# Optimization experiments

Hardware: AMD Instinct MI355X
Metric: run time of the kernel (lower is better)

Reference implementation:

```python
import jax, jax.numpy as jnp
import numpy as np

B, C_IN, C_OUT = 8, 64, 64
H, W = 256, 256
FH, FW = 16, 16  # patch grid from weight map spatial dims
HYPER_PARAMS = C_OUT * C_IN  # kernel_size=1, groups=1


def setup_inputs() -> dict:
    key = jax.random.key(0)
    kx, ks = jax.random.split(key)
    x = jax.random.normal(kx, (B, C_IN, H, W), dtype=jnp.float32)
    # s is the hypernetwork-generated per-patch weight map [b, out*in, fh, fw]
    s = jax.random.normal(ks, (B, HYPER_PARAMS, FH, FW), dtype=jnp.float32)
    return {"x": x, "s": s}


def reference(x, s):
    b, c, h, w = x.shape
    fh, fw = s.shape[-2], s.shape[-1]
    ph, pw = h // fh, w // fw
    out_ch = s.shape[1] // c  # hyper_params = out_ch * c (1x1 kernel, groups=1)
    # weight.permute(0,2,3,1).reshape(b*fh*fw*out, in, 1, 1) -> per-patch [out, in]
    Wp = jnp.transpose(s, (0, 2, 3, 1)).reshape(b, fh, fw, out_ch, c)
    # x.view(b,c,fh,ph,fw,pw).permute(0,2,4,1,3,5) -> per-patch blocks [b,fh,fw,c,ph,pw]
    xp = jnp.transpose(x.reshape(b, c, fh, ph, fw, pw), (0, 2, 4, 1, 3, 5))
    # grouped 1x1 conv over b*fh*fw groups == batched small matmul per patch
    y = jnp.einsum('bijoc,bijcpq->bijopq', Wp, xp)
    # .view(b,fh,fw,-1,ph,pw).permute(0,3,1,4,2,5).reshape(b,-1,h,w)
    return jnp.transpose(y, (0, 3, 1, 4, 2, 5)).reshape(b, out_ch, h, w)
```

## Files before the change

### kernel.cpp

```cpp
#include <hip/hip_runtime.h>

#define NB 8
#define FH 16
#define FW 16

typedef __bf16 bf16x8 __attribute__((ext_vector_type(8)));
typedef float  f32x4  __attribute__((ext_vector_type(4)));

#define WS_BYTES ((size_t)NB * 256 * 512 * 16)

__global__ __launch_bounds__(256) void pack_w_kernel(
    const float* __restrict__ s, bf16x8* __restrict__ ws)
{
    __shared__ float lds[16 * 513];
    const int bid = blockIdx.x;
    const int b   = bid & 7;
    const int pi  = (bid >> 3) & 15;
    const int mt  = (bid >> 7) & 3;
    const int kk  = (bid >> 9) & 1;
    const int tid = threadIdx.x;

    #pragma unroll
    for (int pass = 0; pass < 8; ++pass) {
        const int idx   = pass * 256 + tid;
        const int u     = idx >> 2;
        const int pj4   = idx & 3;
        const int row16 = u >> 5;
        const int cc    = u & 31;
        const size_t row = (size_t)b * 4096 + mt * 1024 + row16 * 64 + kk * 32 + cc;
        const float4 v = *reinterpret_cast<const float4*>(
            s + row * 256 + pi * 16 + pj4 * 4);
        lds[(pj4 * 4 + 0) * 513 + cc * 16 + row16] = v.x;
        lds[(pj4 * 4 + 1) * 513 + cc * 16 + row16] = v.y;
        lds[(pj4 * 4 + 2) * 513 + cc * 16 + row16] = v.z;
        lds[(pj4 * 4 + 3) * 513 + cc * 16 + row16] = v.w;
    }
    __syncthreads();

    const int gl     = tid & 63;
    const int row16  = gl & 15;
    const int lanehi = gl >> 4;
    #pragma unroll
    for (int pjblk = 0; pjblk < 4; ++pjblk) {
        const int pj = pjblk * 4 + (tid >> 6);
        bf16x8 e;
        #pragma unroll
        for (int j = 0; j < 8; ++j)
            e[j] = (__bf16)lds[pj * 513 + (lanehi * 8 + j) * 16 + row16];
        ws[((size_t)(b * 256 + pi * 16 + pj)) * 512 + (mt * 2 + kk) * 64 + gl] = e;
    }
}

__global__ __launch_bounds__(256, 4) void gemm_kernel(
    const float* __restrict__ x,
    const bf16x8* __restrict__ ws,
    float* __restrict__ out)
{
    __shared__ char smem[32768];
    float* smemf = (float*)smem;

    const int bid = blockIdx.x;
    const int b   = bid & 7;
    const int pi  = (bid >> 3) & 15;
    const int ph  = (bid >> 7) & 1;
    const int pjp = (bid >> 8) & 7;
    const int t   = threadIdx.x;
    const int lane = t & 63;
    const int wv   = t >> 6;
    const int pat  = wv & 1;
    const int wrow = wv >> 1;
    const int q    = lane & 15;
    const int hi   = lane >> 4;
    const int w0   = pjp * 32;
    const int row0 = pi * 16 + ph * 8;

    const bf16x8* wbase = ws + ((size_t)(b * 256 + pi * 16 + pjp * 2 + pat)) * 512;
    bf16x8 a[4][2];
    #pragma unroll
    for (int mt = 0; mt < 4; ++mt)
        #pragma unroll
        for (int kk = 0; kk < 2; ++kk)
            a[mt][kk] = wbase[(mt * 2 + kk) * 64 + lane];

    {
        const int swq = lane & 7;
        const int sco = lane >> 3;
        #pragma unroll
        for (int pp = 0; pp < 2; ++pp) {
            const int p = wv * 2 + pp;
            const float* xp = x + ((size_t)(b * 64 + sco * 8)) * 65536
                                + (size_t)(row0 + p) * 256 + w0 + swq * 4;
            f32x4 v[8];
            #pragma unroll
            for (int cc = 0; cc < 8; ++cc)
                v[cc] = *(const f32x4*)(xp + (size_t)cc * 65536);
            #pragma unroll
            for (int i = 0; i < 4; ++i) {
                const int w = swq * 4 + i;
                bf16x8 e;
                #pragma unroll
                for (int cc = 0; cc < 8; ++cc)
                    e[cc] = (__bf16)v[cc][i];
                *(bf16x8*)(smem + p * 4096 + w * 128
                           + ((sco * 16) ^ ((w & 7) << 4) ^ ((p & 7) << 4))) = e;
            }
        }
    }
    __syncthreads();

    bf16x8 bfrag[4][2];
    #pragma unroll
    for (int nt = 0; nt < 4; ++nt) {
        const int p = wrow * 4 + nt;
        const int w = pat * 16 + q;
        #pragma unroll
        for (int kk = 0; kk < 2; ++kk) {
            const int co = kk * 4 + hi;
            bfrag[nt][kk] = *(const bf16x8*)(smem + p * 4096 + w * 128
                            + ((co * 16) ^ ((w & 7) << 4) ^ ((p & 7) << 4)));
        }
    }
    __syncthreads();

    const int u2t = t >> 3;
    const int wq2 = t & 7;
    #pragma unroll
    for (int h = 0; h < 2; ++h) {
        f32x4 acc[2][4];
        #pragma unroll
        for (int m2 = 0; m2 < 2; ++m2)
            #pragma unroll
            for (int nt = 0; nt < 4; ++nt)
                acc[m2][nt] = (f32x4){0.f, 0.f, 0.f, 0.f};

        #pragma unroll
        for (int m2 = 0; m2 < 2; ++m2) {
            const int mt = h * 2 + m2;
            #pragma unroll
            for (int nt = 0; nt < 4; ++nt) {
                acc[m2][nt] = __builtin_amdgcn_mfma_f32_16x16x32_bf16(
                    a[mt][0], bfrag[nt][0], acc[m2][nt], 0, 0, 0);
                acc[m2][nt] = __builtin_amdgcn_mfma_f32_16x16x32_bf16(
                    a[mt][1], bfrag[nt][1], acc[m2][nt], 0, 0, 0);
            }
        }

        #pragma unroll
        for (int m2 = 0; m2 < 2; ++m2)
            #pragma unroll
            for (int nt = 0; nt < 4; ++nt) {
                const int p = wrow * 4 + nt;
                #pragma unroll
                for (int r = 0; r < 4; ++r) {
                    const int o2 = m2 * 16 + hi * 4 + r;
                    const int w  = pat * 16 + q;
                    smemf[(o2 * 8 + p) * 32 + (w ^ ((o2 & 7) << 2))] = acc[m2][nt][r];
                }
            }
        __syncthreads();

        #pragma unroll
        for (int ps = 0; ps < 8; ++ps) {
            const int r2 = ps * 32 + u2t;
            const int o2 = r2 >> 3;
            const int p  = r2 & 7;
            f32x4 vv = *(const f32x4*)&smemf[(o2 * 8 + p) * 32
                                             + ((wq2 * 4) ^ ((o2 & 7) << 2))];
            *(f32x4*)(out + ((size_t)(b * 64 + h * 32 + o2)) * 65536
                          + (size_t)(row0 + p) * 256 + w0 + wq2 * 4) = vv;
        }
        __syncthreads();
    }
}

__global__ __launch_bounds__(512) void hyperpatch_fallback(
    const float* __restrict__ x,
    const float* __restrict__ s,
    float* __restrict__ out)
{
    __shared__ bf16x8 afrag[2][512];
    const int bid = blockIdx.x;
    const int b   = bid >> 7;
    const int pi  = (bid >> 3) & 15;
    const int pj0 = (bid & 7) * 2;
    const int t   = threadIdx.x;
    const int lane = t & 63;
    const int wv   = t >> 6;

    {
        const int g  = t;
        const int mt = g >> 7;
        const int kk = (g >> 6) & 1;
        const int gl = g & 63;
        const int o  = mt * 16 + (gl & 15);
        const int c0 = kk * 32 + (gl >> 4) * 8;
        const float2* sb2 = reinterpret_cast<const float2*>(
            s + ((size_t)b * 4096) * 256 + pi * 16 + pj0);
        bf16x8 ta, tb;
        #pragma unroll
        for (int j = 0; j < 8; ++j) {
            float2 v = sb2[(size_t)(o * 64 + c0 + j) * 128];
            ta[j] = (__bf16)v.x;
            tb[j] = (__bf16)v.y;
        }
        afrag[0][g] = ta;
        afrag[1][g] = tb;
    }

    const int pat  = wv >> 2;
    const int wrow = wv & 3;
    const int q  = lane & 15;
    const int cb = (lane >> 4) * 8;
    const float* xbase = x + (((size_t)b * 64) * 256 + pi * 16) * 256
                           + (pj0 + pat) * 16 + q;
    bf16x8 bfrag[4][2];
    #pragma unroll
    for (int nt = 0; nt < 4; ++nt) {
        const int p = wrow * 4 + nt;
        #pragma unroll
        for (int kk = 0; kk < 2; ++kk) {
            const int c = kk * 32 + cb;
            bf16x8 tv;
            #pragma unroll
            for (int j = 0; j < 8; ++j) {
                float v = xbase[(size_t)(c + j) * 65536 + (size_t)p * 256];
                tv[j] = (__bf16)v;
            }
            bfrag[nt][kk] = tv;
        }
    }

    __syncthreads();

    bf16x8 a[4][2];
    #pragma unroll
    for (int mt = 0; mt < 4; ++mt)
        #pragma unroll
        for (int kk = 0; kk < 2; ++kk)
            a[mt][kk] = afrag[pat][(mt * 2 + kk) * 64 + lane];

    f32x4 acc[4][4];
    #pragma unroll
    for (int mt = 0; mt < 4; ++mt)
        #pragma unroll
        for (int nt = 0; nt < 4; ++nt)
            acc[mt][nt] = (f32x4){0.f, 0.f, 0.f, 0.f};

    #pragma unroll
    for (int mt = 0; mt < 4; ++mt) {
        #pragma unroll
        for (int nt = 0; nt < 4; ++nt) {
            acc[mt][nt] = __builtin_amdgcn_mfma_f32_16x16x32_bf16(
                a[mt][0], bfrag[nt][0], acc[mt][nt], 0, 0, 0);
            acc[mt][nt] = __builtin_amdgcn_mfma_f32_16x16x32_bf16(
                a[mt][1], bfrag[nt][1], acc[mt][nt], 0, 0, 0);
        }
    }

    const int ro = (lane >> 4) * 4;
    float* obase = out + (((size_t)b * 64) * 256 + pi * 16) * 256
                       + (pj0 + pat) * 16 + q;
    #pragma unroll
    for (int mt = 0; mt < 4; ++mt) {
        #pragma unroll
        for (int nt = 0; nt < 4; ++nt) {
            const int p = wrow * 4 + nt;
            #pragma unroll
            for (int r = 0; r < 4; ++r) {
                const int o = mt * 16 + ro + r;
                obase[(size_t)o * 65536 + (size_t)p * 256] = acc[mt][nt][r];
            }
        }
    }
}

extern "C" void kernel_launch(void* const* d_in, const int* in_sizes, int n_in,
                              void* d_out, int out_size, void* d_ws, size_t ws_size,
                              hipStream_t stream)
{
    (void)in_sizes; (void)n_in; (void)out_size;
    const float* x = (const float*)d_in[0];
    const float* s = (const float*)d_in[1];
    float* out = (float*)d_out;

    if (ws_size >= WS_BYTES && d_ws != nullptr) {
        bf16x8* ws = (bf16x8*)d_ws;
        pack_w_kernel<<<dim3(1024), dim3(256), 0, stream>>>(s, ws);
        gemm_kernel<<<dim3(2048), dim3(256), 0, stream>>>(x, ws, out);
    } else {
        hyperpatch_fallback<<<dim3(NB * FH * (FW / 2)), dim3(512), 0, stream>>>(x, s, out);
    }
}
```

Measured before the change: 73.27 us.

## Retile gemm to one full image row per block with streamed weight fragments

Each gemm block now handles one full 256-wide image row of one batch instead of an 8-row by 32-column tile, so x loads and output stores cover whole contiguous rows. Weight fragments for the 16 patches along the row are read from global memory inside the MFMA loop rather than held in registers up front, and launch bounds drop to 3 waves per SIMD. The pack kernel's block index order is also permuted to change its read locality. The row tile reloads the same patch weights once per image row (16 rows per patch row), which adds weight traffic in exchange for longer coalesced x and out accesses.

```diff
diff --git a/kernel.cpp b/kernel.cpp
--- a/kernel.cpp
+++ b/kernel.cpp
@@ -15,9 +15,9 @@
     __shared__ float lds[16 * 513];
     const int bid = blockIdx.x;
     const int b   = bid & 7;
-    const int pi  = (bid >> 3) & 15;
-    const int mt  = (bid >> 7) & 3;
-    const int kk  = (bid >> 9) & 1;
+    const int kk  = (bid >> 3) & 1;
+    const int mt  = (bid >> 4) & 3;
+    const int pi  = (bid >> 6) & 15;
     const int tid = threadIdx.x;
 
     #pragma unroll
@@ -51,7 +51,7 @@
     }
 }
 
-__global__ __launch_bounds__(256, 4) void gemm_kernel(
+__global__ __launch_bounds__(256, 3) void gemm_kernel(
     const float* __restrict__ x,
     const bf16x8* __restrict__ ws,
     float* __restrict__ out)
@@ -61,115 +61,87 @@
 
     const int bid = blockIdx.x;
     const int b   = bid & 7;
-    const int pi  = (bid >> 3) & 15;
-    const int ph  = (bid >> 7) & 1;
-    const int pjp = (bid >> 8) & 7;
+    const int h   = bid >> 3;
+    const int pi  = h >> 4;
     const int t   = threadIdx.x;
     const int lane = t & 63;
     const int wv   = t >> 6;
-    const int pat  = wv & 1;
-    const int wrow = wv >> 1;
     const int q    = lane & 15;
     const int hi   = lane >> 4;
-    const int w0   = pjp * 32;
-    const int row0 = pi * 16 + ph * 8;
-
-    const bf16x8* wbase = ws + ((size_t)(b * 256 + pi * 16 + pjp * 2 + pat)) * 512;
-    bf16x8 a[4][2];
-    #pragma unroll
-    for (int mt = 0; mt < 4; ++mt)
-        #pragma unroll
-        for (int kk = 0; kk < 2; ++kk)
-            a[mt][kk] = wbase[(mt * 2 + kk) * 64 + lane];
 
     {
-        const int swq = lane & 7;
-        const int sco = lane >> 3;
-        #pragma unroll
-        for (int pp = 0; pp < 2; ++pp) {
-            const int p = wv * 2 + pp;
-            const float* xp = x + ((size_t)(b * 64 + sco * 8)) * 65536
-                                + (size_t)(row0 + p) * 256 + w0 + swq * 4;
+        const float* xrow = x + (size_t)b * 64 * 65536 + (size_t)h * 256;
+        #pragma unroll
+        for (int oo = 0; oo < 2; ++oo) {
+            const int co = wv * 2 + oo;
             f32x4 v[8];
             #pragma unroll
             for (int cc = 0; cc < 8; ++cc)
-                v[cc] = *(const f32x4*)(xp + (size_t)cc * 65536);
+                v[cc] = *(const f32x4*)(xrow + (size_t)(co * 8 + cc) * 65536
+                                        + lane * 4);
             #pragma unroll
             for (int i = 0; i < 4; ++i) {
-                const int w = swq * 4 + i;
+                const int w = lane * 4 + i;
                 bf16x8 e;
                 #pragma unroll
                 for (int cc = 0; cc < 8; ++cc)
                     e[cc] = (__bf16)v[cc][i];
-                *(bf16x8*)(smem + p * 4096 + w * 128
-                           + ((sco * 16) ^ ((w & 7) << 4) ^ ((p & 7) << 4))) = e;
-            }
-        }
-    }
-    __syncthreads();
-
-    bf16x8 bfrag[4][2];
-    #pragma unroll
-    for (int nt = 0; nt < 4; ++nt) {
-        const int p = wrow * 4 + nt;
-        const int w = pat * 16 + q;
+                *(bf16x8*)(smem + w * 128 + ((co ^ (w & 7)) * 16)) = e;
+            }
+        }
+    }
+    __syncthreads();
+
+    f32x4 acc[4][4];
+    #pragma unroll
+    for (int j = 0; j < 4; ++j) {
+        const int pj = wv * 4 + j;
+        const bf16x8* wbase = ws + ((size_t)(b * 256 + pi * 16 + pj)) * 512;
+        bf16x8 bf[2];
         #pragma unroll
         for (int kk = 0; kk < 2; ++kk) {
+            const int w  = pj * 16 + q;
             const int co = kk * 4 + hi;
-            bfrag[nt][kk] = *(const bf16x8*)(smem + p * 4096 + w * 128
-                            + ((co * 16) ^ ((w & 7) << 4) ^ ((p & 7) << 4)));
-        }
-    }
-    __syncthreads();
-
-    const int u2t = t >> 3;
-    const int wq2 = t & 7;
-    #pragma unroll
-    for (int h = 0; h < 2; ++h) {
-        f32x4 acc[2][4];
-        #pragma unroll
-        for (int m2 = 0; m2 < 2; ++m2)
-            #pragma unroll
-            for (int nt = 0; nt < 4; ++nt)
-                acc[m2][nt] = (f32x4){0.f, 0.f, 0.f, 0.f};
-
-        #pragma unroll
-        for (int m2 = 0; m2 < 2; ++m2) {
-            const int mt = h * 2 + m2;
-            #pragma unroll
-            for (int nt = 0; nt < 4; ++nt) {
-                acc[m2][nt] = __builtin_amdgcn_mfma_f32_16x16x32_bf16(
-                    a[mt][0], bfrag[nt][0], acc[m2][nt], 0, 0, 0);
-                acc[m2][nt] = __builtin_amdgcn_mfma_f32_16x16x32_bf16(
-                    a[mt][1], bfrag[nt][1], acc[m2][nt], 0, 0, 0);
-            }
-        }
-
-        #pragma unroll
-        for (int m2 = 0; m2 < 2; ++m2)
-            #pragma unroll
-            for (int nt = 0; nt < 4; ++nt) {
-                const int p = wrow * 4 + nt;
+            bf[kk] = *(const bf16x8*)(smem + w * 128 + ((co ^ (w & 7)) * 16));
+        }
+        #pragma unroll
+        for (int mt = 0; mt < 4; ++mt) {
+            acc[j][mt] = (f32x4){0.f, 0.f, 0.f, 0.f};
+            acc[j][mt] = __builtin_amdgcn_mfma_f32_16x16x32_bf16(
+                wbase[(mt * 2 + 0) * 64 + lane], bf[0], acc[j][mt], 0, 0, 0);
+            acc[j][mt] = __builtin_amdgcn_mfma_f32_16x16x32_bf16(
+                wbase[(mt * 2 + 1) * 64 + lane], bf[1], acc[j][mt], 0, 0, 0);
+        }
+        __builtin_amdgcn_sched_barrier(0);
+    }
+    __syncthreads();
+
+    #pragma unroll
+    for (int h2 = 0; h2 < 2; ++h2) {
+        #pragma unroll
+        for (int j = 0; j < 4; ++j) {
+            const int w = (wv * 4 + j) * 16 + q;
+            #pragma unroll
+            for (int m2 = 0; m2 < 2; ++m2) {
+                const int mt = h2 * 2 + m2;
                 #pragma unroll
                 for (int r = 0; r < 4; ++r) {
                     const int o2 = m2 * 16 + hi * 4 + r;
-                    const int w  = pat * 16 + q;
-                    smemf[(o2 * 8 + p) * 32 + (w ^ ((o2 & 7) << 2))] = acc[m2][nt][r];
+                    smemf[o2 * 256 + (w ^ ((o2 & 7) << 2))] = acc[j][mt][r];
                 }
             }
+        }
         __syncthreads();
 
         #pragma unroll
         for (int ps = 0; ps < 8; ++ps) {
-            const int r2 = ps * 32 + u2t;
-            const int o2 = r2 >> 3;
-            const int p  = r2 & 7;
-            f32x4 vv = *(const f32x4*)&smemf[(o2 * 8 + p) * 32
-                                             + ((wq2 * 4) ^ ((o2 & 7) << 2))];
-            *(f32x4*)(out + ((size_t)(b * 64 + h * 32 + o2)) * 65536
-                          + (size_t)(row0 + p) * 256 + w0 + wq2 * 4) = vv;
-        }
-        __syncthreads();
+            const int o2 = ps * 4 + wv;
+            f32x4 vv = *(const f32x4*)&smemf[o2 * 256
+                                             + ((lane * 4) ^ ((o2 & 7) << 2))];
+            *(f32x4*)(out + (size_t)(b * 64 + h2 * 32 + o2) * 65536
+                          + (size_t)h * 256 + lane * 4) = vv;
+        }
+        if (h2 == 0) __syncthreads();
     }
 }
 
```

After: 80.84 us. 10.3% more time.
